# Kernel tuning notes

Hardware: AMD Instinct MI355X
Metric: run time of the kernel (lower is better)

Reference implementation:

```python
import jax, jax.numpy as jnp
import numpy as np

VX = 1.0 / 3.2
VY = 1.0 / 3.2
X_MIN, Y_MIN = -40.0, -20.0
NX, NY = 256, 256  # grid: (40-(-40))/VX, (60-(-20))/VY
X_OFF = VX / 2.0 + X_MIN
Y_OFF = VY / 2.0 + Y_MIN


def setup_inputs() -> dict:
    key = jax.random.key(0)
    ks = jax.random.split(key, 14)
    B = 8
    Ma, Pa, Ca = 60000, 20, 5
    Mr, Pr, Cr = 80000, 32, 3
    Da, Dr, Co = 64, 64, 32
    voxels_agent = jax.random.normal(ks[0], (Ma, Pa, Ca), jnp.float32)
    coors_agent = jnp.stack([
        jax.random.randint(ks[1], (Ma,), 0, B),
        jax.random.randint(ks[2], (Ma,), 0, NY),
        jax.random.randint(ks[3], (Ma,), 0, NX)], axis=-1).astype(jnp.int32)
    num_points_agent = jax.random.randint(ks[4], (Ma,), 1, Pa + 1).astype(jnp.int32)
    voxels_rg = jax.random.normal(ks[5], (Mr, Pr, Cr), jnp.float32)
    coors_rg = jnp.stack([
        jax.random.randint(ks[6], (Mr,), 0, B),
        jax.random.randint(ks[7], (Mr,), 0, NY),
        jax.random.randint(ks[8], (Mr,), 0, NX)], axis=-1).astype(jnp.int32)
    num_points_rg = jax.random.randint(ks[9], (Mr,), 1, Pr + 1).astype(jnp.int32)
    w_agent = 0.02 * jax.random.normal(ks[10], (Ca + 5, Da), jnp.float32)
    b_agent = jnp.zeros((Da,), jnp.float32)
    w_rg = 0.02 * jax.random.normal(ks[11], (Cr + 5, Dr), jnp.float32)
    b_rg = jnp.zeros((Dr,), jnp.float32)
    conv_w = 0.02 * jax.random.normal(ks[12], (3, 3, Da + Dr, Co), jnp.float32)
    conv_b = jnp.zeros((Co,), jnp.float32)
    return dict(voxels_agent=voxels_agent, coors_agent=coors_agent,
                num_points_agent=num_points_agent, voxels_rg=voxels_rg,
                coors_rg=coors_rg, num_points_rg=num_points_rg,
                w_agent=w_agent, b_agent=b_agent, w_rg=w_rg, b_rg=b_rg,
                conv_w=conv_w, conv_b=conv_b, batch_size=B)


def _pillar_vfe(voxels, coors, num_points, W, b):
    # voxels [M,P,C]; coors [M,3]=(batch,y,x); num_points [M]
    M, P, C = voxels.shape
    mask = (jnp.arange(P)[None, :] < num_points[:, None]).astype(voxels.dtype)[..., None]  # [M,P,1]
    npts = jnp.maximum(num_points, 1).astype(voxels.dtype)[:, None, None]
    xyz = voxels[..., :3]
    mean = jnp.sum(xyz * mask, axis=1, keepdims=True) / npts          # pillar cluster mean
    f_cluster = xyz - mean                                            # [M,P,3]
    cx = coors[:, 2].astype(voxels.dtype)[:, None]
    cy = coors[:, 1].astype(voxels.dtype)[:, None]
    f_cx = voxels[..., 0] - (cx * VX + X_OFF)                         # offset from pillar center
    f_cy = voxels[..., 1] - (cy * VY + Y_OFF)
    feats = jnp.concatenate([voxels, f_cluster,
                             jnp.stack([f_cx, f_cy], axis=-1)], axis=-1) * mask  # [M,P,C+5]
    h = jax.nn.relu(feats @ W + b)                                    # [M,P,D]
    return jnp.max(h * mask, axis=1)                                  # [M,D]


def _scatter(feats, coors, B):
    # scatter pillar features into dense BEV canvas [B,NY,NX,D]
    D = feats.shape[1]
    idx = coors[:, 0] * (NY * NX) + coors[:, 1] * NX + coors[:, 2]
    canvas = jnp.zeros((B * NY * NX, D), feats.dtype).at[idx].set(feats)
    return canvas.reshape(B, NY, NX, D)


def reference(voxels_agent, coors_agent, num_points_agent, voxels_rg, coors_rg,
              num_points_rg, w_agent, b_agent, w_rg, b_rg, conv_w, conv_b,
              batch_size):
    pa = _pillar_vfe(voxels_agent, coors_agent, num_points_agent, w_agent, b_agent)
    ca = _scatter(pa, coors_agent, batch_size)
    pr = _pillar_vfe(voxels_rg, coors_rg, num_points_rg, w_rg, b_rg)
    cr = _scatter(pr, coors_rg, batch_size)
    x = jnp.concatenate([ca, cr], axis=-1)                            # [B,NY,NX,128] NHWC
    y = jax.lax.conv_general_dilated(x, conv_w, (1, 1), 'SAME',
                                     dimension_numbers=('NHWC', 'HWIO', 'NHWC'))
    return y + conv_b                                                 # [B,NY,NX,32]
```

## Files before the change

kernel.cpp:

```cpp
#include <hip/hip_runtime.h>
#include <hip/hip_bf16.h>

#define MA 60000
#define PA 20
#define CA 5
#define MR 80000
#define PR 32
#define CR 3
#define NXg 256
#define NYg 256
#define NB 8
#define NCELL (NB * NYg * NXg)

typedef __bf16 bf16x8 __attribute__((ext_vector_type(8)));
typedef float  f32x4  __attribute__((ext_vector_type(4)));
typedef float  f4     __attribute__((ext_vector_type(4)));
typedef float  f2     __attribute__((ext_vector_type(2)));

__device__ __forceinline__ unsigned short f2bf(float f) {
    unsigned int u = __float_as_uint(f);
    u += 0x7fffu + ((u >> 16) & 1u);
    return (unsigned short)(u >> 16);
}

__global__ void __launch_bounds__(256) prep_kernel(int* __restrict__ win,
                                                   const float* __restrict__ conv_w,
                                                   unsigned short* __restrict__ bp) {
    int bid = blockIdx.x, tid = threadIdx.x;
    if (bid < 4096) {
        win[bid * 256 + tid] = -1;
    } else {
        int i = (bid - 4096) * 256 + tid;
        int j    = i & 7;
        int lane = (i >> 3) & 63;
        int nt   = (i >> 9) & 1;
        int kk   = (i >> 10) & 3;
        int tap  = i >> 12;
        int n = nt * 16 + (lane & 15);
        int k = kk * 32 + (lane >> 4) * 8 + j;
        bp[i] = f2bf(conv_w[(tap * 128 + k) * 32 + n]);
    }
}

template <int CIN, int CF, int PMAX, int PMAXp>
__device__ __forceinline__ void vfe_body(
    int bid, const float* __restrict__ vox, const int* __restrict__ coors,
    const int* __restrict__ npts, const float* __restrict__ W,
    const float* __restrict__ bias, unsigned short* __restrict__ feat,
    int* __restrict__ win, int M, int which, f4* sq)
{
    constexpr int PC   = PMAX * CIN;
    constexpr int SR   = PMAXp * CIN;
    constexpr int SR4  = SR / 4;
    constexpr int PP4  = PMAXp / 4;
    constexpr int CPP  = PMAX / 4;

    float* sf = (float*)sq;
    int tid  = threadIdx.x;
    int wv   = tid >> 6;
    int lane = tid & 63;
    int base = bid * 64;
    int cnt  = M - base; cnt = cnt > 64 ? 64 : cnt;

    {
        const f4* gv = (const f4*)vox + (size_t)base * (PC / 4);
        int totc = cnt * CPP;
        for (int c0 = tid; c0 < totc; c0 += 256) {
            int p = c0 / CPP;
            int g = c0 - p * CPP;
            const f4* src = gv + c0 * CIN;
            f4 q[CIN];
#pragma unroll
            for (int t = 0; t < CIN; ++t) q[t] = src[t];
            float* dst = sf + p * SR + g * 4;
#pragma unroll
            for (int cch = 0; cch < CIN; ++cch) {
                f4 w;
#pragma unroll
                for (int j = 0; j < 4; ++j) {
                    int e = j * CIN + cch;
                    w[j] = q[e >> 2][e & 3];
                }
                *(f4*)(dst + cch * PMAXp) = w;
            }
        }
    }

    float wc[CF];
#pragma unroll
    for (int c = 0; c < CF; ++c) wc[c] = W[c * 64 + lane];
    float bd = bias[lane];
    f2 we2[CIN];
    we2[0] = (f2){wc[0] + wc[CIN + 0] + wc[CIN + 3], wc[0] + wc[CIN + 0] + wc[CIN + 3]};
    we2[1] = (f2){wc[1] + wc[CIN + 1] + wc[CIN + 4], wc[1] + wc[CIN + 1] + wc[CIN + 4]};
    we2[2] = (f2){wc[2] + wc[CIN + 2], wc[2] + wc[CIN + 2]};
#pragma unroll
    for (int c = 3; c < CIN; ++c) we2[c] = (f2){wc[c], wc[c]};

    __syncthreads();

    if (tid < cnt) {
        int np = npts[base + tid];
        np = np < 1 ? 1 : (np > PMAX ? PMAX : np);
        int np4 = (np + 3) & ~3;
        float v0[CIN];
#pragma unroll
        for (int c = 0; c < CIN; ++c) v0[c] = sf[tid * SR + c * PMAXp];
        for (int p = np; p < np4; ++p)
#pragma unroll
            for (int c = 0; c < CIN; ++c)
                sf[tid * SR + c * PMAXp + p] = v0[c];
    }
    __syncthreads();

    int np_n = 1, cb_n = 0, cy_n = 0, cx_n = 0;
    if (wv < cnt) {
        np_n = npts[base + wv];
        cb_n = coors[(base + wv) * 3 + 0];
        cy_n = coors[(base + wv) * 3 + 1];
        cx_n = coors[(base + wv) * 3 + 2];
    }

    for (int pi = wv; pi < cnt; pi += 4) {
        int np = np_n, cb = cb_n, cy = cy_n, cx = cx_n;
        int pn = pi + 4;
        if (pn < cnt) {
            np_n = npts[base + pn];
            cb_n = coors[(base + pn) * 3 + 0];
            cy_n = coors[(base + pn) * 3 + 1];
            cx_n = coors[(base + pn) * 3 + 2];
        }
        np = np < 1 ? 1 : (np > PMAX ? PMAX : np);
        int nblk = (np + 3) >> 2;
        float kf = (float)(nblk * 4 - np);

        const f4* pf4 = sq + pi * SR4;
        const float* pf = sf + pi * SR;
        float x0 = pf[0], y0 = pf[PMAXp], z0 = pf[2 * PMAXp];

        f2 sx2 = {0.f, 0.f}, sy2 = {0.f, 0.f}, sz2 = {0.f, 0.f};
        f2 b2  = {-1e30f, -1e30f};

        for (int g = 0; g < nblk; ++g) {
            f4 v[CIN];
#pragma unroll
            for (int c = 0; c < CIN; ++c) v[c] = pf4[c * PP4 + g];
#pragma unroll
            for (int j = 0; j < 2; ++j) {
                f2 x2 = (f2){v[0][2*j], v[0][2*j+1]};
                f2 y2 = (f2){v[1][2*j], v[1][2*j+1]};
                f2 z2 = (f2){v[2][2*j], v[2][2*j+1]};
                sx2 += x2; sy2 += y2; sz2 += z2;
                f2 d2 = x2 * we2[0] + y2 * we2[1] + z2 * we2[2];
#pragma unroll
                for (int c = 3; c < CIN; ++c) {
                    f2 e2 = (f2){v[c][2*j], v[c][2*j+1]};
                    d2 += e2 * we2[c];
                }
                b2 = __builtin_elementwise_max(b2, d2);
            }
        }

        float sx = sx2[0] + sx2[1] - kf * x0;
        float sy = sy2[0] + sy2[1] - kf * y0;
        float sz = sz2[0] + sz2[1] - kf * z0;
        float sbest = fmaxf(b2[0], b2[1]);

        float inv = 1.0f / (float)np;
        float mx = sx * inv, my = sy * inv, mz = sz * inv;
        float xo = (float)cx * 0.3125f + (-39.84375f);
        float yo = (float)cy * 0.3125f + (-19.84375f);
        float off = bd - (mx * wc[CIN + 0] + my * wc[CIN + 1] + mz * wc[CIN + 2])
                       - xo * wc[CIN + 3] - yo * wc[CIN + 4];
        float best = fmaxf(0.0f, sbest + off);

        feat[(size_t)(base + pi) * 64 + lane] = f2bf(best);

        if (lane == 0) {
            atomicMax(&win[((cb * NYg + cy) * NXg + cx) * 2 + which], base + pi);
        }
    }
}

__global__ void __launch_bounds__(256) vfe_all(
    const float* __restrict__ vox_a, const int* __restrict__ coor_a,
    const int* __restrict__ np_a, const float* __restrict__ w_a,
    const float* __restrict__ b_a, unsigned short* __restrict__ feat_a,
    const float* __restrict__ vox_r, const int* __restrict__ coor_r,
    const int* __restrict__ np_r, const float* __restrict__ w_r,
    const float* __restrict__ b_r, unsigned short* __restrict__ feat_r,
    int* __restrict__ win)
{
    __shared__ f4 sq[64 * 25];
    constexpr int NBA = (MA + 63) / 64;
    int bid = blockIdx.x;
    if (bid < NBA)
        vfe_body<CA, CA + 5, PA, 20>(bid, vox_a, coor_a, np_a, w_a, b_a,
                                     feat_a, win, MA, 0, sq);
    else
        vfe_body<CR, CR + 5, PR, 32>(bid - NBA, vox_r, coor_r, np_r, w_r, b_r,
                                     feat_r, win, MR, 1, sq);
}

__global__ void __launch_bounds__(256) conv_kernel(
    const unsigned short* __restrict__ feat_a,
    const unsigned short* __restrict__ feat_r,
    const int2* __restrict__ win2,
    const unsigned short* __restrict__ bpack,
    const float* __restrict__ conv_b,
    float* __restrict__ out)
{
    __shared__ uint4 sA[396 * 5];

    int tid  = threadIdx.x;
    int lane = tid & 63;
    int wv   = tid >> 6;
    int bid  = blockIdx.x;
    int xg = bid & 3, yg = (bid >> 2) & 63, b = bid >> 8;
    int x0 = xg * 64, y0 = yg * 4;
    int mrow = lane & 15, quad = lane >> 4;

    int wA[2] = {-1, -1}, wR[2] = {-1, -1};
#pragma unroll
    for (int r = 0; r < 2; ++r) {
        int cell = tid + r * 256;
        if (cell < 396) {
            int iy = cell / 66, ix = cell - iy * 66;
            int yy = y0 - 1 + iy, xx = x0 - 1 + ix;
            if ((unsigned)yy < 256u && (unsigned)xx < 256u) {
                int2 w2 = win2[(((b << 8) + yy) << 8) + xx];
                wA[r] = w2.x; wR[r] = w2.y;
            }
        }
    }

    f32x4 acc0[4], acc1[4];
#pragma unroll
    for (int mt = 0; mt < 4; ++mt) {
        acc0[mt] = (f32x4){0.f, 0.f, 0.f, 0.f};
        acc1[mt] = (f32x4){0.f, 0.f, 0.f, 0.f};
    }

#pragma unroll
    for (int ph = 0; ph < 4; ++ph) {
        const unsigned short* feat = (ph < 2) ? feat_a : feat_r;
        const int half = (ph & 1) * 32;

#pragma unroll
        for (int r = 0; r < 2; ++r) {
            int cell = tid + r * 256;
            if (cell < 396) {
                int w = (ph < 2) ? wA[r] : wR[r];
                uint4* dst = &sA[cell * 5];
                if (w >= 0) {
                    const uint4* src = (const uint4*)(feat + ((long)w << 6) + half);
                    dst[0] = src[0]; dst[1] = src[1];
                    dst[2] = src[2]; dst[3] = src[3];
                } else {
                    uint4 zz = {0, 0, 0, 0};
                    dst[0] = zz; dst[1] = zz; dst[2] = zz; dst[3] = zz;
                }
            }
        }
        __syncthreads();

#pragma unroll
        for (int tap = 0; tap < 9; ++tap) {
            const int dyo = tap / 3, dxo = tap % 3;
            const unsigned short* bp = bpack + tap * 4096 + ph * 1024 + lane * 8;
            bf16x8 bn0 = *(const bf16x8*)(bp);
            bf16x8 bn1 = *(const bf16x8*)(bp + 512);
            int iy = wv + dyo;
#pragma unroll
            for (int mt = 0; mt < 4; ++mt) {
                int ix = mt * 16 + mrow + dxo;
                bf16x8 a = *(const bf16x8*)(&sA[(iy * 66 + ix) * 5 + quad]);
                acc0[mt] = __builtin_amdgcn_mfma_f32_16x16x32_bf16(a, bn0, acc0[mt], 0, 0, 0);
                acc1[mt] = __builtin_amdgcn_mfma_f32_16x16x32_bf16(a, bn1, acc1[mt], 0, 0, 0);
            }
        }
        __syncthreads();
    }

    int col = lane & 15;
    float bias0 = conv_b[col];
    float bias1 = conv_b[col + 16];
    int cellbase = ((((b << 8) + y0 + wv)) << 8) + x0;
#pragma unroll
    for (int mt = 0; mt < 4; ++mt) {
#pragma unroll
        for (int r = 0; r < 4; ++r) {
            int cell = cellbase + mt * 16 + quad * 4 + r;
            float* o = out + (long)cell * 32;
            o[col]      = acc0[mt][r] + bias0;
            o[col + 16] = acc1[mt][r] + bias1;
        }
    }
}

extern "C" void kernel_launch(void* const* d_in, const int* in_sizes, int n_in,
                              void* d_out, int out_size, void* d_ws, size_t ws_size,
                              hipStream_t stream)
{
    const float* vox_a  = (const float*)d_in[0];
    const int*   coor_a = (const int*)d_in[1];
    const int*   np_a   = (const int*)d_in[2];
    const float* vox_r  = (const float*)d_in[3];
    const int*   coor_r = (const int*)d_in[4];
    const int*   np_r   = (const int*)d_in[5];
    const float* w_a    = (const float*)d_in[6];
    const float* b_a    = (const float*)d_in[7];
    const float* w_r    = (const float*)d_in[8];
    const float* b_r    = (const float*)d_in[9];
    const float* conv_w = (const float*)d_in[10];
    const float* conv_b = (const float*)d_in[11];
    float* out = (float*)d_out;

    char* ws = (char*)d_ws;
    unsigned short* feat_a = (unsigned short*)(ws);
    unsigned short* feat_r = (unsigned short*)(ws + 7680000);
    int* win               = (int*)(ws + 17920000);
    unsigned short* bpack  = (unsigned short*)(ws + 17920000 + 4194304);

    hipLaunchKernelGGL(prep_kernel, dim3(4096 + 144), dim3(256), 0, stream,
                       win, conv_w, bpack);
    hipLaunchKernelGGL(vfe_all, dim3((MA + 63) / 64 + (MR + 63) / 64), dim3(256), 0, stream,
                       vox_a, coor_a, np_a, w_a, b_a, feat_a,
                       vox_r, coor_r, np_r, w_r, b_r, feat_r, win);
    hipLaunchKernelGGL(conv_kernel, dim3(2048), dim3(256), 0, stream,
                       feat_a, feat_r, (const int2*)win, bpack, conv_b, out);
}
```

Baseline: 211.4 us.

## Shrink VFE blocks to 32 pillars and interleave agent/rg blocks; memset winner map

The VFE kernel now runs 128-thread blocks that each handle 32 pillars instead of 256-thread blocks over 64 pillars. Agent and rg blocks are interleaved in a 3:4 pattern so the two pillar types share the GPU evenly rather than running one after the other. The winner-map initialisation moves out of prep_kernel into hipMemsetAsync, which leaves prep_kernel converting only the conv weights. The intent is better occupancy and load balance. The cost is an extra memset operation in the stream and more, smaller blocks.

Result: no change. 212.1 us (+0.3%).

```diff
diff --git a/kernel.cpp b/kernel.cpp
--- a/kernel.cpp
+++ b/kernel.cpp
@@ -23,23 +23,17 @@
     return (unsigned short)(u >> 16);
 }
 
-__global__ void __launch_bounds__(256) prep_kernel(int* __restrict__ win,
-                                                   const float* __restrict__ conv_w,
+__global__ void __launch_bounds__(256) prep_kernel(const float* __restrict__ conv_w,
                                                    unsigned short* __restrict__ bp) {
-    int bid = blockIdx.x, tid = threadIdx.x;
-    if (bid < 4096) {
-        win[bid * 256 + tid] = -1;
-    } else {
-        int i = (bid - 4096) * 256 + tid;
-        int j    = i & 7;
-        int lane = (i >> 3) & 63;
-        int nt   = (i >> 9) & 1;
-        int kk   = (i >> 10) & 3;
-        int tap  = i >> 12;
-        int n = nt * 16 + (lane & 15);
-        int k = kk * 32 + (lane >> 4) * 8 + j;
-        bp[i] = f2bf(conv_w[(tap * 128 + k) * 32 + n]);
-    }
+    int i = blockIdx.x * 256 + threadIdx.x;
+    int j    = i & 7;
+    int lane = (i >> 3) & 63;
+    int nt   = (i >> 9) & 1;
+    int kk   = (i >> 10) & 3;
+    int tap  = i >> 12;
+    int n = nt * 16 + (lane & 15);
+    int k = kk * 32 + (lane >> 4) * 8 + j;
+    bp[i] = f2bf(conv_w[(tap * 128 + k) * 32 + n]);
 }
 
 template <int CIN, int CF, int PMAX, int PMAXp>
@@ -54,18 +48,19 @@
     constexpr int SR4  = SR / 4;
     constexpr int PP4  = PMAXp / 4;
     constexpr int CPP  = PMAX / 4;
+    constexpr int NP   = 32;
 
     float* sf = (float*)sq;
     int tid  = threadIdx.x;
     int wv   = tid >> 6;
     int lane = tid & 63;
-    int base = bid * 64;
-    int cnt  = M - base; cnt = cnt > 64 ? 64 : cnt;
+    int base = bid * NP;
+    int cnt  = M - base; cnt = cnt > NP ? NP : cnt;
 
     {
         const f4* gv = (const f4*)vox + (size_t)base * (PC / 4);
         int totc = cnt * CPP;
-        for (int c0 = tid; c0 < totc; c0 += 256) {
+        for (int c0 = tid; c0 < totc; c0 += 128) {
             int p = c0 / CPP;
             int g = c0 - p * CPP;
             const f4* src = gv + c0 * CIN;
@@ -121,9 +116,9 @@
         cx_n = coors[(base + wv) * 3 + 2];
     }
 
-    for (int pi = wv; pi < cnt; pi += 4) {
+    for (int pi = wv; pi < cnt; pi += 2) {
         int np = np_n, cb = cb_n, cy = cy_n, cx = cx_n;
-        int pn = pi + 4;
+        int pn = pi + 2;
         if (pn < cnt) {
             np_n = npts[base + pn];
             cb_n = coors[(base + pn) * 3 + 0];
@@ -182,7 +177,7 @@
     }
 }
 
-__global__ void __launch_bounds__(256) vfe_all(
+__global__ void __launch_bounds__(128) vfe_all(
     const float* __restrict__ vox_a, const int* __restrict__ coor_a,
     const int* __restrict__ np_a, const float* __restrict__ w_a,
     const float* __restrict__ b_a, unsigned short* __restrict__ feat_a,
@@ -191,14 +186,14 @@
     const float* __restrict__ b_r, unsigned short* __restrict__ feat_r,
     int* __restrict__ win)
 {
-    __shared__ f4 sq[64 * 25];
-    constexpr int NBA = (MA + 63) / 64;
+    __shared__ f4 sq[32 * 25];
     int bid = blockIdx.x;
-    if (bid < NBA)
-        vfe_body<CA, CA + 5, PA, 20>(bid, vox_a, coor_a, np_a, w_a, b_a,
+    int g = bid / 7, r = bid - g * 7;
+    if (r < 3)
+        vfe_body<CA, CA + 5, PA, 20>(g * 3 + r, vox_a, coor_a, np_a, w_a, b_a,
                                      feat_a, win, MA, 0, sq);
     else
-        vfe_body<CR, CR + 5, PR, 32>(bid - NBA, vox_r, coor_r, np_r, w_r, b_r,
+        vfe_body<CR, CR + 5, PR, 32>(g * 4 + (r - 3), vox_r, coor_r, np_r, w_r, b_r,
                                      feat_r, win, MR, 1, sq);
 }
 
@@ -322,9 +317,10 @@
     int* win               = (int*)(ws + 17920000);
     unsigned short* bpack  = (unsigned short*)(ws + 17920000 + 4194304);
 
-    hipLaunchKernelGGL(prep_kernel, dim3(4096 + 144), dim3(256), 0, stream,
-                       win, conv_w, bpack);
-    hipLaunchKernelGGL(vfe_all, dim3((MA + 63) / 64 + (MR + 63) / 64), dim3(256), 0, stream,
+    hipMemsetAsync(win, 0xFF, 2 * (size_t)NCELL * sizeof(int), stream);
+    hipLaunchKernelGGL(prep_kernel, dim3(144), dim3(256), 0, stream,
+                       conv_w, bpack);
+    hipLaunchKernelGGL(vfe_all, dim3(MA / 32 + MR / 32), dim3(128), 0, stream,
                        vox_a, coor_a, np_a, w_a, b_a, feat_a,
                        vox_r, coor_r, np_r, w_r, b_r, feat_r, win);
     hipLaunchKernelGGL(conv_kernel, dim3(2048), dim3(256), 0, stream,
```
